# Kernel optimization log

Hardware: AMD Instinct MI355X
Metric: run time of the kernel (lower is better)

Reference implementation:

```python
import jax, jax.numpy as jnp
import numpy as np

FS = 50000000.0
PI = jnp.pi


def _scale_matrix(alpha, kW, n_pad):
    """kW x kW matrix equal to torch linear-interp (align_corners=False)
    kW -> N -> kW with N = round(kW / clamp(alpha, 0.001)), N bounded by n_pad."""
    a = jnp.maximum(alpha, 0.001)
    N = jnp.clip(jnp.round(kW / a), 1, n_pad).astype(jnp.int32)
    Nf = N.astype(jnp.float32)
    eye_k = jnp.eye(kW, dtype=jnp.float32)
    eye_n = jnp.eye(n_pad, dtype=jnp.float32)
    # down-sample matrix D: length kW -> N (rows j >= N masked to 0)
    j = jnp.arange(n_pad, dtype=jnp.float32)
    c = jnp.maximum((j + 0.5) * (kW / Nf) - 0.5, 0.0)
    i0f = jnp.floor(c)
    w1 = c - i0f
    i0 = jnp.clip(i0f.astype(jnp.int32), 0, kW - 1)
    i1 = jnp.minimum(i0 + 1, kW - 1)
    D = (1.0 - w1)[:, None] * eye_k[i0] + w1[:, None] * eye_k[i1]
    D = D * (jnp.arange(n_pad) < N)[:, None]
    # up-sample matrix U: length N -> kW (reads only cols < N)
    i = jnp.arange(kW, dtype=jnp.float32)
    c2 = jnp.maximum((i + 0.5) * (Nf / kW) - 0.5, 0.0)
    j0 = jnp.floor(c2).astype(jnp.int32)
    j1 = jnp.minimum(j0 + 1, N - 1)
    w2 = c2 - j0.astype(jnp.float32)
    U = (1.0 - w2)[:, None] * eye_n[j0] + w2[:, None] * eye_n[j1]
    return U @ D  # [kW, kW]


def _mix_phase(w, phi):
    # w: [B,OC,2,1,kW], phi: [B,kW]; complex rotation of (I,Q) channel pair
    I, Q = w[:, :, 0, 0, :], w[:, :, 1, 0, :]
    c, sn = jnp.cos(phi)[:, None, :], jnp.sin(phi)[:, None, :]
    return jnp.stack([I * c - Q * sn, I * sn + Q * c], axis=2)[:, :, :, None, :]


def _steered_kernels(z, s, base_w, B):
    OC, IC, _, kW = base_w.shape
    n_pad = 2 * kW
    sf = jnp.nan_to_num(s)
    act = z > 0
    pick = lambda idx, neutral: jnp.where(act[:, idx], sf[:, idx], neutral)
    wB = jnp.broadcast_to(base_w[None], (B, OC, IC, 1, kW))
    # SCALE (PERTURB_ORDER idx 1)
    alpha = pick(1, 1.0)
    M = jax.vmap(lambda a: _scale_matrix(a, kW, n_pad))(alpha)  # [B,kW,kW]
    wB = jnp.einsum('bij,bocuj->bocui', M, wB)
    # CFO (idx 0) then CHIRP (idx 4): sequential phase rotations = summed phase
    n = jnp.arange(kW, dtype=jnp.float32)
    phi = 2.0 * PI * pick(0, 0.0)[:, None] * n[None, :] / FS
    t = n / FS
    phi = phi + PI * pick(4, 0.0)[:, None] * (t ** 2)[None, :]
    wB = _mix_phase(wB, phi)
    # GAIN (idx 2)
    wB = pick(2, 1.0)[:, None, None, None, None] * wB
    # SHIFT (idx 3): per-sample circular roll, out[i] = in[(i - s) mod kW]
    sh = jnp.round(pick(3, 0.0)).astype(jnp.int32)
    idx = (jnp.arange(kW)[None, :] - sh[:, None]) % kW  # [B,kW]
    idx = jnp.broadcast_to(idx[:, None, None, None, :], wB.shape)
    wB = jnp.take_along_axis(wB, idx, axis=-1)
    return wB  # [B,OC,2,1,kW]


def reference(x, z, s, base_w):
    B, IC, _, L = x.shape
    OC, _, _, kW = base_w.shape
    wB = _steered_kernels(z, s, base_w, B)
    xG = x.reshape(1, B * IC, 1, L)
    wG = wB.reshape(B * OC, IC, 1, kW)
    y = jax.lax.conv_general_dilated(
        xG, wG, window_strides=(1, 1), padding=[(0, 0), (kW // 2, kW // 2)],
        dimension_numbers=('NCHW', 'OIHW', 'NCHW'), feature_group_count=B)
    return y.reshape(B, OC, 1, L)


def setup_inputs() -> dict:
    key = jax.random.key(0)
    ks = jax.random.split(key, 4)
    B, OC, IC, kW, L = 32, 64, 2, 65, 65536
    x = jax.random.normal(ks[0], (B, IC, 1, L), dtype=jnp.float32)
    base_w = jax.random.normal(ks[1], (OC, IC, 1, kW), dtype=jnp.float32) * 0.1
    z = jax.random.randint(ks[2], (B, 5), 0, 2).astype(jnp.int32)
    u = jax.random.uniform(ks[3], (B, 5), dtype=jnp.float32)
    f0 = (u[:, 0] * 2.0 - 1.0) * 1.0e5         # CFO in +/-100 kHz
    alpha = 0.75 + u[:, 1] * 0.65               # SCALE in [0.75, 1.4]
    gain = 0.5 + u[:, 2]                        # GAIN in [0.5, 1.5]
    shift = jnp.round((u[:, 3] * 2.0 - 1.0) * 3.0)  # SHIFT integer in [-3, 3]
    chirp = (u[:, 4] * 2.0 - 1.0) * 1.0e12      # CHIRP rate
    s = jnp.stack([f0, alpha, gain, shift, chirp], axis=1)
    return {"x": x, "z": z, "s": s, "base_w": base_w}
```

## Files before the change

kernel.cpp:

```cpp
#include <hip/hip_runtime.h>
#include <math.h>

#define KW 65
#define L_LEN 65536
#define B_N 32
#define OC_N 64
#define KPAD 160
#define SEC 80
#define LT 256
#define NT 8
#define LGRP (LT*NT)
#define XBASE 344

typedef __attribute__((ext_vector_type(8))) short short8;
typedef __attribute__((ext_vector_type(4))) short short4v;
typedef __attribute__((ext_vector_type(4))) float f32x4;

__device__ __forceinline__ unsigned short f2bf(float f) {
    unsigned u = __builtin_bit_cast(unsigned, f);
    unsigned r = u + 0x7FFFu + ((u >> 16) & 1u);
    return (unsigned short)(r >> 16);
}

__device__ __forceinline__ float nan0(float v) {
    if (isnan(v)) return 0.0f;
    if (isinf(v)) return v > 0.0f ? 3.4028234663852886e38f : -3.4028234663852886e38f;
    return v;
}

__global__ __launch_bounds__(256) void steer_weights(
        const int* __restrict__ z, const float* __restrict__ s,
        const float* __restrict__ bw, unsigned short* __restrict__ wpk) {
    const float PI = 3.14159265358979323846f;
    const float FS = 50000000.0f;
    int ocg = blockIdx.x;
    int b   = blockIdx.y;
    int t   = threadIdx.x;

    const int*   zb = z + b * 5;
    const float* sb = s + b * 5;
    float f0    = (zb[0] > 0) ? nan0(sb[0]) : 0.0f;
    float alpha = (zb[1] > 0) ? nan0(sb[1]) : 1.0f;
    float gain  = (zb[2] > 0) ? nan0(sb[2]) : 1.0f;
    float shf   = (zb[3] > 0) ? nan0(sb[3]) : 0.0f;
    float chirp = (zb[4] > 0) ? nan0(sb[4]) : 0.0f;

    float a = fmaxf(alpha, 0.001f);
    float Nf_raw = rintf(65.0f / a);
    int   N  = (int)fminf(fmaxf(Nf_raw, 1.0f), 130.0f);
    float Nf = (float)N;
    int   sh = (int)rintf(shf);

    __shared__ float rw[8][2][KW];
    __shared__ float cph[KW], sph[KW];
    __shared__ int   j0t[KW], j1t[KW];
    __shared__ float w2t[KW];
    __shared__ int   i0t[130], i1t[130];
    __shared__ float w1t[130];

    if (t < KW) {
        float n  = (float)t;
        float tt = n / FS;
        float phi = 2.0f * PI * f0 * n / FS + PI * chirp * tt * tt;
        cph[t] = cosf(phi);
        sph[t] = sinf(phi);
        float c2  = fmaxf(((float)t + 0.5f) * (Nf / 65.0f) - 0.5f, 0.0f);
        float j0f = floorf(c2);
        j0t[t] = (int)j0f;
        j1t[t] = min((int)j0f + 1, N - 1);
        w2t[t] = c2 - j0f;
    } else if (t < KW + 130) {
        int j = t - KW;
        float c   = fmaxf(((float)j + 0.5f) * (65.0f / Nf) - 0.5f, 0.0f);
        float i0f = floorf(c);
        int   i0  = min((int)i0f, KW - 1);
        i0t[j] = i0;
        i1t[j] = min(i0 + 1, KW - 1);
        w1t[j] = c - i0f;
    }
    __syncthreads();

    for (int item = t; item < 16 * KW; item += 256) {
        int row = item / KW, i = item % KW;
        const float* w = bw + (((ocg * 8 + (row >> 1)) * 2) + (row & 1)) * KW;
        int j0 = j0t[i], j1 = j1t[i];
        float v0 = (1.0f - w1t[j0]) * w[i0t[j0]] + w1t[j0] * w[i1t[j0]];
        float v1 = (1.0f - w1t[j1]) * w[i0t[j1]] + w1t[j1] * w[i1t[j1]];
        rw[row >> 1][row & 1][i] = (1.0f - w2t[i]) * v0 + w2t[i] * v1;
    }
    __syncthreads();

    int sh0 = ((sh % KW) + KW) % KW;
    for (int item = t; item < 8 * KW; item += 256) {
        int ocl = item / KW, k = item % KW;
        unsigned short* ob = wpk + ((size_t)b * OC_N + ocg * 8 + ocl) * KPAD;
        float I = rw[ocl][0][k], Q = rw[ocl][1][k];
        float cp = cph[k], sp = sph[k];
        float Ip = (I * cp - Q * sp) * gain;
        float Qp = (I * sp + Q * cp) * gain;
        int kk = k + sh0; if (kk >= KW) kk -= KW;
        ob[kk]       = f2bf(Ip);
        ob[SEC + kk] = f2bf(Qp);
    }
    for (int item = t; item < 8 * 30; item += 256) {
        int ocl = item / 30, rem = item % 30;
        int sec = rem / 15, kk = KW + rem % 15;
        unsigned short* ob = wpk + ((size_t)b * OC_N + ocg * 8 + ocl) * KPAD;
        ob[sec * SEC + kk] = 0;
    }
}

__global__ __launch_bounds__(256, 3) void steer_conv_mfma(
        const float* __restrict__ x, const unsigned short* __restrict__ wpk,
        float* __restrict__ y) {
    int b   = blockIdx.y;
    int L0  = blockIdx.x * LGRP;
    int tid = threadIdx.x;
    int wv = tid >> 6, lane = tid & 63;
    int c = lane & 15, g = lane >> 4;
    int a = wv & 1, lsub = wv >> 1;

    __shared__ __align__(16) unsigned short xt[2][4][2][XBASE];

    short8 afr[2][5];
    #pragma unroll
    for (int ot = 0; ot < 2; ++ot) {
        const unsigned short* wb = wpk + ((size_t)b * OC_N + 32 * a + 16 * ot + c) * KPAD;
        #pragma unroll
        for (int s = 0; s < 5; ++s)
            afr[ot][s] = *(const short8*)(wb + 32 * s + 8 * g);
    }

    const float* xb = x + (size_t)b * 2 * L_LEN;

    bool isLoader = (tid >= 84);
    int lidx = tid - 84;
    int lch = lidx / 86, li4 = lidx % 86;

    int boff[5];
    #pragma unroll
    for (int s = 0; s < 5; ++s) {
        int k0 = 32 * s + 8 * g;
        int ch = (k0 >= SEC) ? 1 : 0;
        int t0 = k0 - SEC * ch;
        boff[s] = ch * XBASE + 128 * lsub + t0;
    }

    auto loadwin = [&](int l0) -> float4 {
        int gi = l0 - 32 + 4 * li4;
        float4 v;
        if (gi >= 0 && gi + 3 < L_LEN) {
            v = *(const float4*)(xb + (size_t)lch * L_LEN + gi);
        } else {
            float tmp[4];
            #pragma unroll
            for (int u = 0; u < 4; ++u) {
                int q = gi + u;
                tmp[u] = (q >= 0 && q < L_LEN) ? xb[(size_t)lch * L_LEN + q] : 0.0f;
            }
            v = make_float4(tmp[0], tmp[1], tmp[2], tmp[3]);
        }
        return v;
    };

    float4 v = make_float4(0.f, 0.f, 0.f, 0.f);
    if (isLoader) v = loadwin(L0);

    int cur = 0;
    for (int t = 0; t < NT; ++t) {
        int l0 = L0 + t * LT;
        if (isLoader) {
            unsigned r0 = (unsigned)f2bf(v.x) | ((unsigned)f2bf(v.y) << 16);
            unsigned r1 = (unsigned)f2bf(v.z) | ((unsigned)f2bf(v.w) << 16);
            *(uint2*)&xt[cur][0][lch][4 * li4] = make_uint2(r0, r1);
        }
        __syncthreads();
        if (tid < 84) {
            int ch = tid / 42, j = tid % 42;
            const unsigned* src = (const unsigned*)&xt[cur][0][ch][8 * j];
            unsigned d[8];
            #pragma unroll
            for (int i = 0; i < 8; ++i) d[i] = src[i];
            #pragma unroll
            for (int p = 1; p < 4; ++p) {
                int q = p >> 1;
                unsigned o[4];
                #pragma unroll
                for (int i = 0; i < 4; ++i)
                    o[i] = (p & 1) ? ((d[i + q] >> 16) | (d[i + q + 1] << 16)) : d[i + q];
                *(uint4*)&xt[cur][p][ch][8 * j] = make_uint4(o[0], o[1], o[2], o[3]);
            }
        } else if (t + 1 < NT) {
            v = loadwin(l0 + LT);
        }
        __syncthreads();

        f32x4 acc[2][2][4];
        #pragma unroll
        for (int ot = 0; ot < 2; ++ot)
            #pragma unroll
            for (int q = 0; q < 2; ++q)
                #pragma unroll
                for (int p = 0; p < 4; ++p) acc[ot][q][p] = (f32x4){0.f, 0.f, 0.f, 0.f};

        #pragma unroll
        for (int q = 0; q < 2; ++q) {
            #pragma unroll
            for (int p = 0; p < 4; ++p) {
                const unsigned short* xp = &xt[cur][p][0][0] + 64 * q + 4 * c;
                #pragma unroll
                for (int s = 0; s < 5; ++s) {
                    union { short4v h[2]; short8 v8; } u;
                    u.h[0] = *(const short4v*)(xp + boff[s]);
                    u.h[1] = *(const short4v*)(xp + boff[s] + 4);
                    short8 bfr = u.v8;
                    acc[0][q][p] = __builtin_amdgcn_mfma_f32_16x16x32_bf16(afr[0][s], bfr, acc[0][q][p], 0, 0, 0);
                    acc[1][q][p] = __builtin_amdgcn_mfma_f32_16x16x32_bf16(afr[1][s], bfr, acc[1][q][p], 0, 0, 0);
                }
            }
        }

        #pragma unroll
        for (int ot = 0; ot < 2; ++ot) {
            #pragma unroll
            for (int q = 0; q < 2; ++q) {
                #pragma unroll
                for (int r = 0; r < 4; ++r) {
                    int oc = 32 * a + 16 * ot + 4 * g + r;
                    float* yr = y + ((size_t)b * OC_N + oc) * L_LEN + l0 + 128 * lsub + 64 * q + 4 * c;
                    *(f32x4*)yr = (f32x4){ acc[ot][q][0][r], acc[ot][q][1][r],
                                           acc[ot][q][2][r], acc[ot][q][3][r] };
                }
            }
        }
        cur ^= 1;
    }
}

extern "C" void kernel_launch(void* const* d_in, const int* in_sizes, int n_in,
                              void* d_out, int out_size, void* d_ws, size_t ws_size,
                              hipStream_t stream) {
    const float* x  = (const float*)d_in[0];
    const int*   z  = (const int*)d_in[1];
    const float* s  = (const float*)d_in[2];
    const float* bw = (const float*)d_in[3];
    float* y = (float*)d_out;
    unsigned short* wpk = (unsigned short*)d_ws;

    steer_weights<<<dim3(8, B_N), dim3(256), 0, stream>>>(z, s, bw, wpk);
    steer_conv_mfma<<<dim3(L_LEN / LGRP, B_N), dim3(256), 0, stream>>>(x, wpk, y);
}
```

Baseline: 135.5 us.

## Halve conv block to two waves with smaller tile and wider loader stores

```diff
diff --git a/kernel.cpp b/kernel.cpp
--- a/kernel.cpp
+++ b/kernel.cpp
@@ -7,10 +7,10 @@
 #define OC_N 64
 #define KPAD 160
 #define SEC 80
-#define LT 256
+#define LT 128
 #define NT 8
 #define LGRP (LT*NT)
-#define XBASE 344
+#define XW 216
 
 typedef __attribute__((ext_vector_type(8))) short short8;
 typedef __attribute__((ext_vector_type(4))) short short4v;
@@ -20,6 +20,10 @@
     unsigned u = __builtin_bit_cast(unsigned, f);
     unsigned r = u + 0x7FFFu + ((u >> 16) & 1u);
     return (unsigned short)(r >> 16);
+}
+
+__device__ __forceinline__ unsigned pk2(float a, float b) {
+    return (unsigned)f2bf(a) | ((unsigned)f2bf(b) << 16);
 }
 
 __device__ __forceinline__ float nan0(float v) {
@@ -110,7 +114,7 @@
     }
 }
 
-__global__ __launch_bounds__(256, 3) void steer_conv_mfma(
+__global__ __launch_bounds__(128, 3) void steer_conv_mfma(
         const float* __restrict__ x, const unsigned short* __restrict__ wpk,
         float* __restrict__ y) {
     int b   = blockIdx.y;
@@ -118,9 +122,9 @@
     int tid = threadIdx.x;
     int wv = tid >> 6, lane = tid & 63;
     int c = lane & 15, g = lane >> 4;
-    int a = wv & 1, lsub = wv >> 1;
-
-    __shared__ __align__(16) unsigned short xt[2][4][2][XBASE];
+    int a = wv;
+
+    __shared__ __align__(16) unsigned short xt[2][4][2][XW];
 
     short8 afr[2][5];
     #pragma unroll
@@ -133,9 +137,8 @@
 
     const float* xb = x + (size_t)b * 2 * L_LEN;
 
-    bool isLoader = (tid >= 84);
-    int lidx = tid - 84;
-    int lch = lidx / 86, li4 = lidx % 86;
+    bool isLdr = (tid >= 52 && tid < 106);
+    int lch = (tid - 52) / 27, li8 = (tid - 52) % 27;
 
     int boff[5];
     #pragma unroll
@@ -143,40 +146,39 @@
         int k0 = 32 * s + 8 * g;
         int ch = (k0 >= SEC) ? 1 : 0;
         int t0 = k0 - SEC * ch;
-        boff[s] = ch * XBASE + 128 * lsub + t0;
-    }
-
-    auto loadwin = [&](int l0) -> float4 {
-        int gi = l0 - 32 + 4 * li4;
-        float4 v;
-        if (gi >= 0 && gi + 3 < L_LEN) {
-            v = *(const float4*)(xb + (size_t)lch * L_LEN + gi);
-        } else {
-            float tmp[4];
-            #pragma unroll
-            for (int u = 0; u < 4; ++u) {
-                int q = gi + u;
-                tmp[u] = (q >= 0 && q < L_LEN) ? xb[(size_t)lch * L_LEN + q] : 0.0f;
-            }
-            v = make_float4(tmp[0], tmp[1], tmp[2], tmp[3]);
-        }
-        return v;
+        boff[s] = ch * XW + t0;
+    }
+
+    auto ldf4 = [&](int gi) -> float4 {
+        if (gi >= 0 && gi + 3 < L_LEN)
+            return *(const float4*)(xb + (size_t)lch * L_LEN + gi);
+        float tmp[4];
+        #pragma unroll
+        for (int u = 0; u < 4; ++u) {
+            int q = gi + u;
+            tmp[u] = (q >= 0 && q < L_LEN) ? xb[(size_t)lch * L_LEN + q] : 0.0f;
+        }
+        return make_float4(tmp[0], tmp[1], tmp[2], tmp[3]);
     };
 
-    float4 v = make_float4(0.f, 0.f, 0.f, 0.f);
-    if (isLoader) v = loadwin(L0);
+    float4 va = make_float4(0.f, 0.f, 0.f, 0.f), vb = va;
+    if (isLdr) {
+        int gi0 = L0 - 32 + 8 * li8;
+        va = ldf4(gi0);
+        vb = ldf4(gi0 + 4);
+    }
 
     int cur = 0;
     for (int t = 0; t < NT; ++t) {
         int l0 = L0 + t * LT;
-        if (isLoader) {
-            unsigned r0 = (unsigned)f2bf(v.x) | ((unsigned)f2bf(v.y) << 16);
-            unsigned r1 = (unsigned)f2bf(v.z) | ((unsigned)f2bf(v.w) << 16);
-            *(uint2*)&xt[cur][0][lch][4 * li4] = make_uint2(r0, r1);
+        if (isLdr) {
+            uint4 o = make_uint4(pk2(va.x, va.y), pk2(va.z, va.w),
+                                 pk2(vb.x, vb.y), pk2(vb.z, vb.w));
+            *(uint4*)&xt[cur][0][lch][8 * li8] = o;
         }
         __syncthreads();
-        if (tid < 84) {
-            int ch = tid / 42, j = tid % 42;
+        if (tid < 52) {
+            int ch = tid / 26, j = tid % 26;
             const unsigned* src = (const unsigned*)&xt[cur][0][ch][8 * j];
             unsigned d[8];
             #pragma unroll
@@ -190,8 +192,10 @@
                     o[i] = (p & 1) ? ((d[i + q] >> 16) | (d[i + q + 1] << 16)) : d[i + q];
                 *(uint4*)&xt[cur][p][ch][8 * j] = make_uint4(o[0], o[1], o[2], o[3]);
             }
-        } else if (t + 1 < NT) {
-            v = loadwin(l0 + LT);
+        } else if (isLdr && t + 1 < NT) {
+            int gi0 = l0 + LT - 32 + 8 * li8;
+            va = ldf4(gi0);
+            vb = ldf4(gi0 + 4);
         }
         __syncthreads();
 
@@ -227,7 +231,7 @@
                 #pragma unroll
                 for (int r = 0; r < 4; ++r) {
                     int oc = 32 * a + 16 * ot + 4 * g + r;
-                    float* yr = y + ((size_t)b * OC_N + oc) * L_LEN + l0 + 128 * lsub + 64 * q + 4 * c;
+                    float* yr = y + ((size_t)b * OC_N + oc) * L_LEN + l0 + 64 * q + 4 * c;
                     *(f32x4*)yr = (f32x4){ acc[ot][q][0][r], acc[ot][q][1][r],
                                            acc[ot][q][2][r], acc[ot][q][3][r] };
                 }
@@ -248,5 +252,5 @@
     unsigned short* wpk = (unsigned short*)d_ws;
 
     steer_weights<<<dim3(8, B_N), dim3(256), 0, stream>>>(z, s, bw, wpk);
-    steer_conv_mfma<<<dim3(L_LEN / LGRP, B_N), dim3(256), 0, stream>>>(x, wpk, y);
-}
+    steer_conv_mfma<<<dim3(L_LEN / LGRP, B_N), dim3(128), 0, stream>>>(x, wpk, y);
+}
```

Result: slower. 166.3 us (+22.8%).
